# Kernel optimization log

Measured on AMD Instinct MI355X. Metric: run time of the kernel, lower is better.

## Reference

```python
import jax, jax.numpy as jnp
import numpy as np

UNITS = 2048
INPUT_DIM = 2048
BATCH = 8192


def setup_inputs() -> dict:
    key = jax.random.key(0)
    k_x, k_w = jax.random.split(key)
    inputs = jax.random.normal(k_x, (BATCH, INPUT_DIM), dtype=jnp.float32)
    # random_normal initializer in keras defaults to stddev=0.05
    w = jax.random.normal(k_w, (INPUT_DIM, UNITS), dtype=jnp.float32) * 0.05
    b = jnp.zeros((UNITS,), dtype=jnp.float32)
    return {"inputs": inputs, "w": w, "b": b}


def reference(inputs, w, b):
    # matmul + bias
    result = jnp.matmul(inputs, w) + b  # [B, units]
    # per-row: if first element > 0.5, add 1 to whole row, else subtract 1
    cond = result[:, :1] > 0.5  # [B, 1], broadcasts over row
    return jnp.where(cond, result + 1.0, result - 1.0)
```

## Files before the change

kernel.cpp:

```cpp
#include <hip/hip_runtime.h>
#include <hip/hip_bf16.h>
#include <stdint.h>

#define M_DIM 8192
#define N_DIM 2048
#define K_DIM 2048

typedef __attribute__((ext_vector_type(8))) short bf16x8;
typedef __attribute__((ext_vector_type(8))) short short8;
typedef __attribute__((ext_vector_type(4))) float f32x4;

static __device__ __forceinline__ unsigned short f2bf(float f) {
  union { float f; unsigned u; } a; a.f = f;
  unsigned u = a.u;
  u += 0x7FFFu + ((u >> 16) & 1u);
  return (unsigned short)(u >> 16);
}

static __device__ __forceinline__ void async16(void* lds, const void* g) {
  __builtin_amdgcn_global_load_lds(
      (const __attribute__((address_space(1))) unsigned int*)g,
      (__attribute__((address_space(3))) unsigned int*)lds, 16, 0, 0);
}

#define BAR()                                \
  do {                                       \
    asm volatile("" ::: "memory");           \
    __builtin_amdgcn_s_barrier();            \
    asm volatile("" ::: "memory");           \
  } while (0)
#define VMCNT(n) asm volatile("s_waitcnt vmcnt(" #n ")" ::: "memory")

__global__ __launch_bounds__(256) void k_wcol(const float* __restrict__ W,
                                              float* __restrict__ wcol) {
  int k = blockIdx.x * 256 + threadIdx.x;
  if (k < K_DIM) wcol[k] = W[(size_t)k * N_DIM];
}

__global__ __launch_bounds__(256) void k_convX(const float* __restrict__ X,
    const float* __restrict__ wcol, const float* __restrict__ b,
    unsigned short* __restrict__ Xb, float* __restrict__ adj) {
  const int m = blockIdx.x;
  const int t = threadIdx.x;
  const float4* xr = (const float4*)(X + (size_t)m * K_DIM);
  const float4* wc = (const float4*)wcol;
  float4 x0 = xr[2 * t], x1 = xr[2 * t + 1];
  float4 w0 = wc[2 * t], w1 = wc[2 * t + 1];
  short8 o;
  o[0] = (short)f2bf(x0.x); o[1] = (short)f2bf(x0.y);
  o[2] = (short)f2bf(x0.z); o[3] = (short)f2bf(x0.w);
  o[4] = (short)f2bf(x1.x); o[5] = (short)f2bf(x1.y);
  o[6] = (short)f2bf(x1.z); o[7] = (short)f2bf(x1.w);
  *(short8*)(Xb + (size_t)m * K_DIM + t * 8) = o;
  double s = (double)x0.x * w0.x + (double)x0.y * w0.y +
             (double)x0.z * w0.z + (double)x0.w * w0.w +
             (double)x1.x * w1.x + (double)x1.y * w1.y +
             (double)x1.z * w1.z + (double)x1.w * w1.w;
  #pragma unroll
  for (int off = 32; off > 0; off >>= 1) s += __shfl_down(s, off, 64);
  __shared__ double red[4];
  if ((t & 63) == 0) red[t >> 6] = s;
  __syncthreads();
  if (t == 0) {
    double tot = red[0] + red[1] + red[2] + red[3] + (double)b[0];
    adj[m] = (tot > 0.5) ? 1.0f : -1.0f;
  }
}

__global__ __launch_bounds__(256) void k_transW(const float* __restrict__ W,
                                                unsigned short* __restrict__ Wt) {
  __shared__ float tile[64][65];
  const int bx = blockIdx.x & 31;
  const int by = blockIdx.x >> 5;
  const int n0 = bx * 64, k0 = by * 64;
  const int t = threadIdx.x;
  #pragma unroll
  for (int i = 0; i < 16; ++i) {
    int lin = i * 256 + t;
    int r = lin >> 6, c = lin & 63;
    tile[r][c] = W[(size_t)(k0 + r) * N_DIM + n0 + c];
  }
  __syncthreads();
  #pragma unroll
  for (int i = 0; i < 16; ++i) {
    int lin = i * 256 + t;
    int r = lin >> 6, c = lin & 63;
    Wt[(size_t)(n0 + r) * K_DIM + k0 + c] = f2bf(tile[c][r]);
  }
}

__device__ __forceinline__ void stage_unit(char* ldsc,
    const unsigned short* __restrict__ src, int row0, int kt,
    int isB, int sel, int wid, int l) {
  char* base = ldsc + (size_t)(kt & 1) * 65536 + (size_t)isB * 32768;
  #pragma unroll
  for (int j = 0; j < 2; ++j) {
    int s = wid * 2 + j;
    int sub_c = s & 1;
    int idx = s >> 1;
    int sub_r = isB ? ((idx & 1) + (idx >> 1) * 4 + sel * 2)
                    : ((idx & 3) + ((idx & 4) ? 8 : 0) + sel * 4);
    int grow = row0 + sub_r * 16 + (l >> 2);
    int gcol = kt * 64 + sub_c * 32 + (((l & 3) * 8) ^ ((l & 32) >> 1));
    async16(base + (size_t)(sub_r * 2 + sub_c) * 1024,
            src + (size_t)grow * K_DIM + gcol);
  }
}

__global__ __launch_bounds__(512, 1) void k_gemm8(
    const unsigned short* __restrict__ A,
    const unsigned short* __restrict__ B,
    const float* __restrict__ bias,
    const float* __restrict__ adj,
    float* __restrict__ out) {
  __shared__ unsigned short lds[2 * 2 * 256 * 64];
  char* ldsc = (char*)lds;

  const int t = threadIdx.x;
  const int wid = t >> 6, l = t & 63;
  const int wm = wid >> 2, wn = wid & 3;

  const int bid = blockIdx.x;
  const int swz = (bid & 7) * 32 + (bid >> 3);
  const int bm = swz >> 3, bn = swz & 7;
  const int m0 = bm * 256, n0 = bn * 256;

  const int r = l & 15, q = l >> 4;
  const int rdoff = (r * 64 + q * 16) ^ ((r & 8) << 2);

  f32x4 acc[8][4] = {};

#define STG(isB, sel, kt) \
  stage_unit(ldsc, (isB) ? B : A, (isB) ? n0 : m0, kt, isB, sel, wid, l)

#define PHASE(BUF, MH, NH, STAGE_STMT, WAIT_STMT)                          \
  {                                                                        \
    const char* ab = ldsc + (size_t)(BUF) * 65536;                         \
    const char* bb = ab + 32768;                                           \
    bf16x8 af[2][4];                                                       \
    bf16x8 bv[2][2];                                                       \
    _Pragma("unroll") for (int mi4 = 0; mi4 < 4; ++mi4) {                  \
      int sub_r = wm * 8 + (MH) * 4 + mi4;                                 \
      _Pragma("unroll") for (int ks = 0; ks < 2; ++ks)                     \
        af[ks][mi4] =                                                      \
            *(const bf16x8*)(ab + (size_t)(sub_r * 2 + ks) * 1024 + rdoff);\
    }                                                                      \
    _Pragma("unroll") for (int ni2 = 0; ni2 < 2; ++ni2) {                  \
      int sub_r = wn * 4 + (NH) * 2 + ni2;                                 \
      _Pragma("unroll") for (int ks = 0; ks < 2; ++ks)                     \
        bv[ks][ni2] =                                                      \
            *(const bf16x8*)(bb + (size_t)(sub_r * 2 + ks) * 1024 + rdoff);\
    }                                                                      \
    STAGE_STMT;                                                            \
    BAR();                                                                 \
    __builtin_amdgcn_s_setprio(1);                                         \
    _Pragma("unroll") for (int mi4 = 0; mi4 < 4; ++mi4)                    \
      _Pragma("unroll") for (int ni2 = 0; ni2 < 2; ++ni2) {                \
        const int mi = (MH) * 4 + mi4, ni = (NH) * 2 + ni2;                \
        acc[mi][ni] = __builtin_amdgcn_mfma_f32_16x16x32_bf16(             \
            af[0][mi4], bv[0][ni2], acc[mi][ni], 0, 0, 0);                 \
        acc[mi][ni] = __builtin_amdgcn_mfma_f32_16x16x32_bf16(             \
            af[1][mi4], bv[1][ni2], acc[mi][ni], 0, 0, 0);                 \
      }                                                                    \
    __builtin_amdgcn_s_setprio(0);                                         \
    WAIT_STMT;                                                             \
    BAR();                                                                 \
  }

  STG(0, 0, 0); STG(1, 0, 0); STG(1, 1, 0); STG(0, 1, 0);
  VMCNT(0);
  BAR();

  for (int j = 0; j < 31; ++j) {
    const int buf = j & 1;
    const int nt = j + 1;
    PHASE(buf, 0, 0, STG(0, 0, nt), VMCNT(4));
    PHASE(buf, 0, 1, STG(1, 0, nt), VMCNT(4));
    PHASE(buf, 1, 0, STG(1, 1, nt), );
    PHASE(buf, 1, 1, STG(0, 1, nt), VMCNT(4));
  }
  PHASE(1, 0, 0, , VMCNT(2));
  PHASE(1, 0, 1, , VMCNT(0));
  PHASE(1, 1, 0, , );
  PHASE(1, 1, 1, , );

#undef PHASE
#undef STG

  #pragma unroll
  for (int mi = 0; mi < 8; ++mi) {
    const int rowb = m0 + wm * 128 + mi * 16 + q * 4;
    float adjv[4];
    #pragma unroll
    for (int j = 0; j < 4; ++j) adjv[j] = adj[rowb + j];
    #pragma unroll
    for (int ni = 0; ni < 4; ++ni) {
      const int col = n0 + wn * 64 + ni * 16 + r;
      const float bvs = bias[col];
      #pragma unroll
      for (int j = 0; j < 4; ++j)
        out[(size_t)(rowb + j) * N_DIM + col] = acc[mi][ni][j] + bvs + adjv[j];
    }
  }
}

__global__ __launch_bounds__(256) void k_gemm_f32(const float* __restrict__ X,
    const float* __restrict__ W, const float* __restrict__ b,
    float* __restrict__ out) {
  __shared__ float As[16][16];
  __shared__ float Bs[16][17];
  const int bn = blockIdx.x & 127, bm = blockIdx.x >> 7;
  const int tx = threadIdx.x & 15, ty = threadIdx.x >> 4;
  const int row = bm * 16 + ty, col = bn * 16 + tx;
  float acc = 0.f;
  for (int k0 = 0; k0 < K_DIM; k0 += 16) {
    As[ty][tx] = X[(size_t)row * K_DIM + k0 + tx];
    Bs[ty][tx] = W[(size_t)(k0 + ty) * N_DIM + col];
    __syncthreads();
    #pragma unroll
    for (int kk = 0; kk < 16; ++kk) acc += As[ty][kk] * Bs[kk][tx];
    __syncthreads();
  }
  out[(size_t)row * N_DIM + col] = acc + b[col];
}

__global__ __launch_bounds__(256) void k_rowadj(float* __restrict__ out) {
  const int m = blockIdx.x;
  const float c0 = out[(size_t)m * N_DIM];
  __syncthreads();
  const float a = (c0 > 0.5f) ? 1.0f : -1.0f;
  for (int n = threadIdx.x; n < N_DIM; n += 256)
    out[(size_t)m * N_DIM + n] += a;
}

extern "C" void kernel_launch(void* const* d_in, const int* in_sizes, int n_in,
                              void* d_out, int out_size, void* d_ws, size_t ws_size,
                              hipStream_t stream) {
  const float* X = (const float*)d_in[0];
  const float* W = (const float*)d_in[1];
  const float* b = (const float*)d_in[2];
  float* out = (float*)d_out;

  const size_t XB_OFF   = 0;
  const size_t WT_OFF   = (size_t)M_DIM * K_DIM * 2;
  const size_t ADJ_OFF  = WT_OFF + (size_t)N_DIM * K_DIM * 2;
  const size_t WCOL_OFF = ADJ_OFF + (size_t)M_DIM * 4;
  const size_t NEED     = WCOL_OFF + (size_t)K_DIM * 4;

  if (ws_size >= NEED) {
    unsigned short* Xb  = (unsigned short*)((char*)d_ws + XB_OFF);
    unsigned short* Wt  = (unsigned short*)((char*)d_ws + WT_OFF);
    float* adj  = (float*)((char*)d_ws + ADJ_OFF);
    float* wcol = (float*)((char*)d_ws + WCOL_OFF);
    k_wcol<<<dim3(8), dim3(256), 0, stream>>>(W, wcol);
    k_convX<<<dim3(M_DIM), dim3(256), 0, stream>>>(X, wcol, b, Xb, adj);
    k_transW<<<dim3(1024), dim3(256), 0, stream>>>(W, Wt);
    k_gemm8<<<dim3((M_DIM / 256) * (N_DIM / 256)), dim3(512), 0, stream>>>(
        Xb, Wt, b, adj, out);
  } else {
    k_gemm_f32<<<dim3((M_DIM / 16) * (N_DIM / 16)), dim3(256), 0, stream>>>(
        X, W, b, out);
    k_rowadj<<<dim3(M_DIM), dim3(256), 0, stream>>>(out);
  }
}
```

Baseline: 100.5 us.

## Reuse LDS fragments across phases and relax vmcnt waits in GEMM pipeline

The A and B fragments are now read from LDS once per k-tile and kept in registers across the four phases, instead of being reloaded each phase. A is read twice per tile and B once, which cuts LDS read traffic. The vmcnt waits are also relaxed (VMCNT(2) in the prologue, a shifted wait schedule in the loop) so more global-to-LDS loads stay in flight. This raises register pressure, and the looser waits carry a correctness risk if a phase reads a staged unit before its load has landed.

```diff
diff --git a/kernel.cpp b/kernel.cpp
--- a/kernel.cpp
+++ b/kernel.cpp
@@ -133,58 +133,69 @@
 #define STG(isB, sel, kt) \
   stage_unit(ldsc, (isB) ? B : A, (isB) ? n0 : m0, kt, isB, sel, wid, l)
 
-#define PHASE(BUF, MH, NH, STAGE_STMT, WAIT_STMT)                          \
+#define RD_A(MH)                                                           \
+  _Pragma("unroll") for (int mi4 = 0; mi4 < 4; ++mi4) {                    \
+    const int sub_r = wm * 8 + (MH) * 4 + mi4;                             \
+    _Pragma("unroll") for (int ks = 0; ks < 2; ++ks)                       \
+      af[ks][mi4] =                                                        \
+          *(const bf16x8*)(ab + (size_t)(sub_r * 2 + ks) * 1024 + rdoff);  \
+  }
+
+#define RD_B(DST, NH)                                                      \
+  _Pragma("unroll") for (int ni2 = 0; ni2 < 2; ++ni2) {                    \
+    const int sub_r = wn * 4 + (NH) * 2 + ni2;                             \
+    _Pragma("unroll") for (int ks = 0; ks < 2; ++ks)                       \
+      DST[ks][ni2] =                                                       \
+          *(const bf16x8*)(bb + (size_t)(sub_r * 2 + ks) * 1024 + rdoff);  \
+  }
+
+#define PHASE(BUF, MH, NH, READ_STMT, STAGE_STMT, WAIT_STMT)               \
   {                                                                        \
     const char* ab = ldsc + (size_t)(BUF) * 65536;                         \
     const char* bb = ab + 32768;                                           \
-    bf16x8 af[2][4];                                                       \
-    bf16x8 bv[2][2];                                                       \
-    _Pragma("unroll") for (int mi4 = 0; mi4 < 4; ++mi4) {                  \
-      int sub_r = wm * 8 + (MH) * 4 + mi4;                                 \
-      _Pragma("unroll") for (int ks = 0; ks < 2; ++ks)                     \
-        af[ks][mi4] =                                                      \
-            *(const bf16x8*)(ab + (size_t)(sub_r * 2 + ks) * 1024 + rdoff);\
-    }                                                                      \
-    _Pragma("unroll") for (int ni2 = 0; ni2 < 2; ++ni2) {                  \
-      int sub_r = wn * 4 + (NH) * 2 + ni2;                                 \
-      _Pragma("unroll") for (int ks = 0; ks < 2; ++ks)                     \
-        bv[ks][ni2] =                                                      \
-            *(const bf16x8*)(bb + (size_t)(sub_r * 2 + ks) * 1024 + rdoff);\
-    }                                                                      \
+    (void)ab; (void)bb;                                                    \
+    READ_STMT;                                                             \
     STAGE_STMT;                                                            \
     BAR();                                                                 \
     __builtin_amdgcn_s_setprio(1);                                         \
-    _Pragma("unroll") for (int mi4 = 0; mi4 < 4; ++mi4)                    \
-      _Pragma("unroll") for (int ni2 = 0; ni2 < 2; ++ni2) {                \
-        const int mi = (MH) * 4 + mi4, ni = (NH) * 2 + ni2;                \
-        acc[mi][ni] = __builtin_amdgcn_mfma_f32_16x16x32_bf16(             \
-            af[0][mi4], bv[0][ni2], acc[mi][ni], 0, 0, 0);                 \
-        acc[mi][ni] = __builtin_amdgcn_mfma_f32_16x16x32_bf16(             \
-            af[1][mi4], bv[1][ni2], acc[mi][ni], 0, 0, 0);                 \
-      }                                                                    \
+    _Pragma("unroll") for (int ks = 0; ks < 2; ++ks)                       \
+      _Pragma("unroll") for (int mi4 = 0; mi4 < 4; ++mi4)                  \
+        _Pragma("unroll") for (int ni2 = 0; ni2 < 2; ++ni2) {              \
+          const int mi = (MH) * 4 + mi4, ni = (NH) * 2 + ni2;              \
+          acc[mi][ni] = __builtin_amdgcn_mfma_f32_16x16x32_bf16(           \
+              af[ks][mi4], ((NH) ? bv1 : bv0)[ks][ni2], acc[mi][ni],       \
+              0, 0, 0);                                                    \
+        }                                                                  \
     __builtin_amdgcn_s_setprio(0);                                         \
     WAIT_STMT;                                                             \
     BAR();                                                                 \
   }
 
   STG(0, 0, 0); STG(1, 0, 0); STG(1, 1, 0); STG(0, 1, 0);
-  VMCNT(0);
+  VMCNT(2);
   BAR();
 
   for (int j = 0; j < 31; ++j) {
     const int buf = j & 1;
     const int nt = j + 1;
-    PHASE(buf, 0, 0, STG(0, 0, nt), VMCNT(4));
-    PHASE(buf, 0, 1, STG(1, 0, nt), VMCNT(4));
-    PHASE(buf, 1, 0, STG(1, 1, nt), );
-    PHASE(buf, 1, 1, STG(0, 1, nt), VMCNT(4));
-  }
-  PHASE(1, 0, 0, , VMCNT(2));
-  PHASE(1, 0, 1, , VMCNT(0));
-  PHASE(1, 1, 0, , );
-  PHASE(1, 1, 1, , );
+    bf16x8 af[2][4], bv0[2][2], bv1[2][2];
+    PHASE(buf, 0, 0, RD_A(0); RD_B(bv0, 0); RD_B(bv1, 1),
+          STG(0, 0, nt), );
+    PHASE(buf, 0, 1, , STG(1, 0, nt), VMCNT(4));
+    PHASE(buf, 1, 0, RD_A(1), STG(1, 1, nt), );
+    PHASE(buf, 1, 1, , STG(0, 1, nt), VMCNT(2));
+  }
+  {
+    bf16x8 af[2][4], bv0[2][2], bv1[2][2];
+    PHASE(1, 0, 0, RD_A(0); RD_B(bv0, 0); RD_B(bv1, 1), , );
+    PHASE(1, 0, 1, , , VMCNT(0));
+    PHASE(1, 1, 0, RD_A(1), , );
+    PHASE(1, 1, 1, , , );
+  }
 
 #undef PHASE
+#undef RD_A
+#undef RD_B
 #undef STG
 
   #pragma unroll
```

After: 93.20 us. 7.3% less time.

## Reuse LDS fragments across GEMM phases, deepen prefetch, fold wcol into transpose

Applied to the files above, without the earlier changes.

The GEMM main loop now keeps A and B fragments in registers across the four sub-phases, so each K tile reads A halves and B halves from LDS once instead of re-reading them per phase. The global-to-LDS staging schedule is also shifted: two stage units of the next tile are issued before the first barrier, with adjusted vmcnt waits and an explicit lgkmcnt wait before the MFMAs. The separate k_wcol launch is removed and its work folded into the W transpose kernel, dropping one launch. The explicit waits and the changed staging order depend on correct buffer-hazard reasoning, and holding more fragments raises register pressure.

```diff
diff --git a/kernel.cpp b/kernel.cpp
--- a/kernel.cpp
+++ b/kernel.cpp
@@ -30,11 +30,35 @@
     asm volatile("" ::: "memory");           \
   } while (0)
 #define VMCNT(n) asm volatile("s_waitcnt vmcnt(" #n ")" ::: "memory")
-
-__global__ __launch_bounds__(256) void k_wcol(const float* __restrict__ W,
-                                              float* __restrict__ wcol) {
-  int k = blockIdx.x * 256 + threadIdx.x;
-  if (k < K_DIM) wcol[k] = W[(size_t)k * N_DIM];
+#define LGK()                                                \
+  do {                                                       \
+    asm volatile("s_waitcnt lgkmcnt(0)" ::: "memory");       \
+    __builtin_amdgcn_sched_barrier(0);                       \
+  } while (0)
+
+__global__ __launch_bounds__(256) void k_transW(const float* __restrict__ W,
+                                                unsigned short* __restrict__ Wt,
+                                                float* __restrict__ wcol) {
+  __shared__ float tile[64][65];
+  const int bx = blockIdx.x & 31;
+  const int by = blockIdx.x >> 5;
+  const int n0 = bx * 64, k0 = by * 64;
+  const int t = threadIdx.x;
+  #pragma unroll
+  for (int i = 0; i < 16; ++i) {
+    int lin = i * 256 + t;
+    int r = lin >> 6, c = lin & 63;
+    float v = W[(size_t)(k0 + r) * N_DIM + n0 + c];
+    tile[r][c] = v;
+    if (bx == 0 && c == 0) wcol[k0 + r] = v;
+  }
+  __syncthreads();
+  #pragma unroll
+  for (int i = 0; i < 16; ++i) {
+    int lin = i * 256 + t;
+    int r = lin >> 6, c = lin & 63;
+    Wt[(size_t)(n0 + r) * K_DIM + k0 + c] = f2bf(tile[c][r]);
+  }
 }
 
 __global__ __launch_bounds__(256) void k_convX(const float* __restrict__ X,
@@ -67,28 +91,6 @@
   }
 }
 
-__global__ __launch_bounds__(256) void k_transW(const float* __restrict__ W,
-                                                unsigned short* __restrict__ Wt) {
-  __shared__ float tile[64][65];
-  const int bx = blockIdx.x & 31;
-  const int by = blockIdx.x >> 5;
-  const int n0 = bx * 64, k0 = by * 64;
-  const int t = threadIdx.x;
-  #pragma unroll
-  for (int i = 0; i < 16; ++i) {
-    int lin = i * 256 + t;
-    int r = lin >> 6, c = lin & 63;
-    tile[r][c] = W[(size_t)(k0 + r) * N_DIM + n0 + c];
-  }
-  __syncthreads();
-  #pragma unroll
-  for (int i = 0; i < 16; ++i) {
-    int lin = i * 256 + t;
-    int r = lin >> 6, c = lin & 63;
-    Wt[(size_t)(n0 + r) * K_DIM + k0 + c] = f2bf(tile[c][r]);
-  }
-}
-
 __device__ __forceinline__ void stage_unit(char* ldsc,
     const unsigned short* __restrict__ src, int row0, int kt,
     int isB, int sel, int wid, int l) {
@@ -128,63 +130,87 @@
   const int r = l & 15, q = l >> 4;
   const int rdoff = (r * 64 + q * 16) ^ ((r & 8) << 2);
 
+  const char* ab0 = ldsc;
+  const char* bb0 = ldsc + 32768;
+  const char* ab1 = ldsc + 65536;
+  const char* bb1 = ldsc + 98304;
+
   f32x4 acc[8][4] = {};
+  bf16x8 af0[2][4], af1[2][4], bv0[2][2], bv1[2][2];
 
 #define STG(isB, sel, kt) \
   stage_unit(ldsc, (isB) ? B : A, (isB) ? n0 : m0, kt, isB, sel, wid, l)
 
-#define PHASE(BUF, MH, NH, STAGE_STMT, WAIT_STMT)                          \
-  {                                                                        \
-    const char* ab = ldsc + (size_t)(BUF) * 65536;                         \
-    const char* bb = ab + 32768;                                           \
-    bf16x8 af[2][4];                                                       \
-    bf16x8 bv[2][2];                                                       \
-    _Pragma("unroll") for (int mi4 = 0; mi4 < 4; ++mi4) {                  \
-      int sub_r = wm * 8 + (MH) * 4 + mi4;                                 \
-      _Pragma("unroll") for (int ks = 0; ks < 2; ++ks)                     \
-        af[ks][mi4] =                                                      \
-            *(const bf16x8*)(ab + (size_t)(sub_r * 2 + ks) * 1024 + rdoff);\
-    }                                                                      \
-    _Pragma("unroll") for (int ni2 = 0; ni2 < 2; ++ni2) {                  \
-      int sub_r = wn * 4 + (NH) * 2 + ni2;                                 \
-      _Pragma("unroll") for (int ks = 0; ks < 2; ++ks)                     \
-        bv[ks][ni2] =                                                      \
-            *(const bf16x8*)(bb + (size_t)(sub_r * 2 + ks) * 1024 + rdoff);\
-    }                                                                      \
-    STAGE_STMT;                                                            \
-    BAR();                                                                 \
-    __builtin_amdgcn_s_setprio(1);                                         \
-    _Pragma("unroll") for (int mi4 = 0; mi4 < 4; ++mi4)                    \
-      _Pragma("unroll") for (int ni2 = 0; ni2 < 2; ++ni2) {                \
-        const int mi = (MH) * 4 + mi4, ni = (NH) * 2 + ni2;                \
-        acc[mi][ni] = __builtin_amdgcn_mfma_f32_16x16x32_bf16(             \
-            af[0][mi4], bv[0][ni2], acc[mi][ni], 0, 0, 0);                 \
-        acc[mi][ni] = __builtin_amdgcn_mfma_f32_16x16x32_bf16(             \
-            af[1][mi4], bv[1][ni2], acc[mi][ni], 0, 0, 0);                 \
-      }                                                                    \
-    __builtin_amdgcn_s_setprio(0);                                         \
-    WAIT_STMT;                                                             \
-    BAR();                                                                 \
+#define RD_A(DST, MH, AB)                                                   \
+  _Pragma("unroll") for (int mi4 = 0; mi4 < 4; ++mi4) {                     \
+    const int sub_r = wm * 8 + (MH) * 4 + mi4;                              \
+    _Pragma("unroll") for (int ks = 0; ks < 2; ++ks)                        \
+      DST[ks][mi4] =                                                        \
+          *(const bf16x8*)((AB) + (size_t)(sub_r * 2 + ks) * 1024 + rdoff); \
+  }
+
+#define RD_B(DST, NH, BB)                                                   \
+  _Pragma("unroll") for (int ni2 = 0; ni2 < 2; ++ni2) {                     \
+    const int sub_r = wn * 4 + (NH) * 2 + ni2;                              \
+    _Pragma("unroll") for (int ks = 0; ks < 2; ++ks)                        \
+      DST[ks][ni2] =                                                        \
+          *(const bf16x8*)((BB) + (size_t)(sub_r * 2 + ks) * 1024 + rdoff); \
+  }
+
+#define CL(MH, NH, AF, BV)                                                  \
+  __builtin_amdgcn_s_setprio(1);                                            \
+  _Pragma("unroll") for (int ks = 0; ks < 2; ++ks)                          \
+    _Pragma("unroll") for (int mi4 = 0; mi4 < 4; ++mi4)                     \
+      _Pragma("unroll") for (int ni2 = 0; ni2 < 2; ++ni2)                   \
+        acc[(MH) * 4 + mi4][(NH) * 2 + ni2] =                               \
+            __builtin_amdgcn_mfma_f32_16x16x32_bf16(                        \
+                AF[ks][mi4], BV[ks][ni2],                                   \
+                acc[(MH) * 4 + mi4][(NH) * 2 + ni2], 0, 0, 0);              \
+  __builtin_amdgcn_s_setprio(0);
+
+#define PH(RD_STMT, STG_STMT, CL_STMT, WAIT_STMT)                           \
+  {                                                                         \
+    RD_STMT;                                                                \
+    STG_STMT;                                                               \
+    BAR();                                                                  \
+    LGK();                                                                  \
+    CL_STMT;                                                                \
+    WAIT_STMT;                                                              \
+    BAR();                                                                  \
   }
 
   STG(0, 0, 0); STG(1, 0, 0); STG(1, 1, 0); STG(0, 1, 0);
-  VMCNT(0);
+  STG(0, 0, 1); STG(1, 0, 1);
+  VMCNT(4);
   BAR();
 
-  for (int j = 0; j < 31; ++j) {
-    const int buf = j & 1;
-    const int nt = j + 1;
-    PHASE(buf, 0, 0, STG(0, 0, nt), VMCNT(4));
-    PHASE(buf, 0, 1, STG(1, 0, nt), VMCNT(4));
-    PHASE(buf, 1, 0, STG(1, 1, nt), );
-    PHASE(buf, 1, 1, STG(0, 1, nt), VMCNT(4));
-  }
-  PHASE(1, 0, 0, , VMCNT(2));
-  PHASE(1, 0, 1, , VMCNT(0));
-  PHASE(1, 1, 0, , );
-  PHASE(1, 1, 1, , );
-
-#undef PHASE
+  for (int i = 0; i < 15; ++i) {
+    const int t1 = 2 * i + 1, t2 = 2 * i + 2, t3 = 2 * i + 3;
+    PH(RD_A(af0, 0, ab0); RD_B(bv0, 0, bb0), STG(1, 1, t1),
+       CL(0, 0, af0, bv0), );
+    PH(RD_B(bv1, 1, bb0), STG(0, 1, t1), CL(0, 1, af0, bv1), );
+    PH(RD_A(af1, 1, ab0), STG(0, 0, t2), CL(1, 0, af1, bv0), );
+    PH(, STG(1, 0, t2), CL(1, 1, af1, bv1), VMCNT(4));
+    PH(RD_A(af0, 0, ab1); RD_B(bv0, 0, bb1), STG(1, 1, t2),
+       CL(0, 0, af0, bv0), );
+    PH(RD_B(bv1, 1, bb1), STG(0, 1, t2), CL(0, 1, af0, bv1), );
+    PH(RD_A(af1, 1, ab1), STG(0, 0, t3), CL(1, 0, af1, bv0), );
+    PH(, STG(1, 0, t3), CL(1, 1, af1, bv1), VMCNT(4));
+  }
+  PH(RD_A(af0, 0, ab0); RD_B(bv0, 0, bb0), STG(1, 1, 31),
+     CL(0, 0, af0, bv0), );
+  PH(RD_B(bv1, 1, bb0), STG(0, 1, 31), CL(0, 1, af0, bv1), );
+  PH(RD_A(af1, 1, ab0), , CL(1, 0, af1, bv0), );
+  PH(, , CL(1, 1, af1, bv1), VMCNT(0));
+  PH(RD_A(af0, 0, ab1); RD_B(bv0, 0, bb1), , CL(0, 0, af0, bv0), );
+  PH(RD_B(bv1, 1, bb1), , CL(0, 1, af0, bv1), );
+  PH(RD_A(af1, 1, ab1), , CL(1, 0, af1, bv0), );
+  PH(, , CL(1, 1, af1, bv1), );
+
+#undef PH
+#undef CL
+#undef RD_A
+#undef RD_B
 #undef STG
 
   #pragma unroll
@@ -252,9 +278,8 @@
     unsigned short* Wt  = (unsigned short*)((char*)d_ws + WT_OFF);
     float* adj  = (float*)((char*)d_ws + ADJ_OFF);
     float* wcol = (float*)((char*)d_ws + WCOL_OFF);
-    k_wcol<<<dim3(8), dim3(256), 0, stream>>>(W, wcol);
+    k_transW<<<dim3(1024), dim3(256), 0, stream>>>(W, Wt, wcol);
     k_convX<<<dim3(M_DIM), dim3(256), 0, stream>>>(X, wcol, b, Xb, adj);
-    k_transW<<<dim3(1024), dim3(256), 0, stream>>>(W, Wt);
     k_gemm8<<<dim3((M_DIM / 256) * (N_DIM / 256)), dim3(512), 0, stream>>>(
         Xb, Wt, b, adj, out);
   } else {
```

Result: faster. 91.14 us (-9.3%).
